# Kernel tuning notes

Hardware: AMD Instinct MI355X
Metric: run time of the kernel (lower is better)

The kernel has to match this reference:

```python
import jax, jax.numpy as jnp
import numpy as np

B, T, N, D = 256, 200, 8, 64
MODEL = N * D          # 512
FFN_H = 1024 * N // 4  # 2048
EPS = 1.1920929e-07    # torch.finfo(float32).eps (nn.RMSNorm default eps=None)


def setup_inputs() -> dict:
    key = jax.random.key(0)
    ks = jax.random.split(key, 9)
    def xavier(k, shape):
        fan_in, fan_out = shape[-2], shape[-1]
        lim = float(np.sqrt(6.0 / (fan_in + fan_out)))
        return jax.random.uniform(k, shape, jnp.float32, -lim, lim)
    q = jax.random.normal(ks[0], (B, N, D), jnp.float32)
    seq = jax.random.normal(ks[1], (B, T, MODEL), jnp.float32)
    seq_mask = jax.random.randint(ks[2], (B, T), 0, 2) > 0
    seq_mask = seq_mask.at[:, 0].set(True)  # ensure >=1 valid position per row
    return {
        "q": q,
        "seq": seq,
        "rms_w": jnp.ones((MODEL,), jnp.float32),
        "w1": xavier(ks[3], (MODEL, FFN_H)),
        "w2": xavier(ks[4], (MODEL, FFN_H)),
        "w3": xavier(ks[5], (FFN_H, MODEL)),
        "w_k": xavier(ks[6], (N, D, D)),
        "w_v": xavier(ks[7], (N, D, D)),
        "seq_mask": seq_mask,
    }


def reference(q, seq, rms_w, w1, w2, w3, w_k, w_v, seq_mask):
    # RMSNorm
    sn = seq * jax.lax.rsqrt(jnp.mean(seq * seq, axis=-1, keepdims=True) + EPS) * rms_w
    # SwiGLU FFN + residual (dropout=0 / eval)
    h = (jax.nn.silu(sn @ w1) * (sn @ w2)) @ w3 + seq  # (B,T,N*D)
    hh = h.reshape(B, T, N, D)
    keys = jnp.einsum('btnd,nde->bnte', hh, w_k)    # (B,N,T,D)
    values = jnp.einsum('btnd,nde->bnte', hh, w_v)  # (B,N,T,D)
    scale = D ** (-0.5)
    scores = jnp.einsum('bnd,bntd->bnt', q, keys) * scale  # single-query attention
    scores = jnp.where(seq_mask[:, None, :], scores, -jnp.inf)
    attn = jax.nn.softmax(scores, axis=-1)
    ctx = jnp.einsum('bnt,bntd->bnd', attn, values)
    return ctx + q
```

## Files before the change

kernel.cpp:

```cpp
#include <hip/hip_runtime.h>
#include <hip/hip_fp16.h>
#include <cstdint>
#include <cstddef>

typedef unsigned short u16t;
typedef __bf16 bf16x8 __attribute__((ext_vector_type(8)));
typedef float f32x4 __attribute__((ext_vector_type(4)));
typedef unsigned short u16x8 __attribute__((ext_vector_type(8)));

#define BT_ROWS 51200
#define MODEL 512
#define FFNH 2048

__device__ __forceinline__ float bf2f(u16t u) {
  union { unsigned int i; float f; } v; v.i = ((unsigned int)u) << 16; return v.f;
}
__device__ __forceinline__ u16t f2bf(float f) {
  union { float f; unsigned int i; } v; v.f = f;
  return (u16t)((v.i + 0x7fffu + ((v.i >> 16) & 1u)) >> 16);
}
__device__ __forceinline__ float ldf(const void* p, size_t i, int dt) {
  if (dt == 1) return ((const float*)p)[i];
  u16t u = ((const u16t*)p)[i];
  if (dt == 0) return bf2f(u);
  __half h; *(u16t*)&h = u; return __half2float(h);
}
__device__ __forceinline__ void stf(void* p, size_t i, int dt, float f) {
  if (dt == 1) { ((float*)p)[i] = f; }
  else if (dt == 0) { ((u16t*)p)[i] = f2bf(f); }
  else { __half h = __float2half(f); ((u16t*)p)[i] = *(u16t*)&h; }
}
__device__ __forceinline__ void gl2lds16(const void* g, void* l) {
  __builtin_amdgcn_global_load_lds((const __attribute__((address_space(1))) void*)g,
                                   (__attribute__((address_space(3))) void*)l, 16, 0, 0);
}

__global__ __launch_bounds__(256) void detect_dtype_k(const unsigned int* __restrict__ w1,
                                                      int* __restrict__ dflag) {
  __shared__ int sh[8];
  int a = 0, bc = 0;
  for (int it = 0; it < 64; it++) {
    unsigned int w = w1[it * 256 + threadIdx.x];
    u16t lo = (u16t)(w & 0xffffu), hi = (u16t)(w >> 16);
    float flo = bf2f(lo);
    a += (!(fabsf(flo) < 0.25f)) ? 1 : 0;
    __half hh; *(u16t*)&hh = hi; float fhi = __half2float(hh);
    bc += (fabsf(fhi) > 0.25f && fabsf(fhi) < 256.f) ? 1 : 0;
  }
#pragma unroll
  for (int o = 32; o; o >>= 1) { a += __shfl_xor(a, o); bc += __shfl_xor(bc, o); }
  int w = threadIdx.x >> 6;
  if ((threadIdx.x & 63) == 0) { sh[w] = a; sh[4 + w] = bc; }
  __syncthreads();
  if (threadIdx.x == 0) {
    int A = sh[0] + sh[1] + sh[2] + sh[3];
    int B = sh[4] + sh[5] + sh[6] + sh[7];
    dflag[0] = (A > 256) ? 1 : ((B < 256) ? 2 : 0);
  }
}

__global__ __launch_bounds__(256) void detect_mask_k(const unsigned int* __restrict__ msk,
                                                     int* __restrict__ flag) {
  int i = blockIdx.x * 256 + threadIdx.x;
  int bad = 0;
  if (i < 12800) bad = (msk[i] > 1u) ? 1 : 0;
  unsigned long long bl = __ballot(bad);
  if ((threadIdx.x & 63) == 0 && bl) atomicOr(flag, 1);
}

__global__ __launch_bounds__(256) void rmsnorm_k(const void* __restrict__ seq,
                                                 const void* __restrict__ w,
                                                 const int* __restrict__ dfp,
                                                 u16t* __restrict__ xn) {
  const int dt = dfp[0];
  int row = blockIdx.x * 4 + (threadIdx.x >> 6);
  int lane = threadIdx.x & 63;
  size_t base = (size_t)row * MODEL + lane * 8;
  float x[8]; float ss = 0.f;
  if (dt == 0) {
    u16x8 xv = *(const u16x8*)((const u16t*)seq + base);
#pragma unroll
    for (int j = 0; j < 8; j++) { x[j] = bf2f(xv[j]); ss += x[j] * x[j]; }
  } else if (dt == 1) {
    const f32x4* p = (const f32x4*)((const float*)seq + base);
    f32x4 va = p[0], vb = p[1];
#pragma unroll
    for (int j = 0; j < 4; j++) { x[j] = va[j]; x[4 + j] = vb[j]; }
#pragma unroll
    for (int j = 0; j < 8; j++) ss += x[j] * x[j];
  } else {
#pragma unroll
    for (int j = 0; j < 8; j++) { x[j] = ldf(seq, base + j, dt); ss += x[j] * x[j]; }
  }
#pragma unroll
  for (int o = 32; o; o >>= 1) ss += __shfl_xor(ss, o);
  float rstd = rsqrtf(ss * (1.f / 512.f) + 1.1920929e-07f);
  u16x8 ov;
#pragma unroll
  for (int j = 0; j < 8; j++) ov[j] = f2bf(x[j] * rstd * ldf(w, lane * 8 + j, dt));
  *(u16x8*)(xn + base) = ov;
}

__global__ __launch_bounds__(256) void transpose_k(const void* __restrict__ src,
                                                   u16t* __restrict__ dst,
                                                   const int* __restrict__ dfp,
                                                   int R, int C) {
  const int dt = dfp[0];
  __shared__ u16t tile[32][33];
  int x = threadIdx.x & 31, y = threadIdx.x >> 5;
  int c0 = blockIdx.x * 32, r0 = blockIdx.y * 32;
#pragma unroll
  for (int i = 0; i < 32; i += 8)
    tile[y + i][x] = f2bf(ldf(src, (size_t)(r0 + y + i) * C + c0 + x, dt));
  __syncthreads();
#pragma unroll
  for (int i = 0; i < 32; i += 8) dst[(size_t)(c0 + y + i) * R + r0 + x] = tile[x][y + i];
}


__global__ __launch_bounds__(256, 4) void ffn_gemm1(const u16t* __restrict__ Xn,
                                                    const u16t* __restrict__ W1t,
                                                    const u16t* __restrict__ W2t,
                                                    u16t* __restrict__ Act) {
  __shared__ u16t As[128 * 64];
  __shared__ u16t B1s[64 * 64];
  __shared__ u16t B2s[64 * 64];
  const int tid = threadIdx.x;
  const int lane = tid & 63;
  const int wave = tid >> 6;
  const int wr = wave >> 1, wc = wave & 1;
  const int quad = lane >> 4, l16 = lane & 15;
  const int nBase = blockIdx.x * 64;
  const int mBase = blockIdx.y * 128;
  const int wuBase = tid & ~63;

  f32x4 acc1[4][2], acc2[4][2];
  const f32x4 zf = {0.f, 0.f, 0.f, 0.f};
#pragma unroll
  for (int i = 0; i < 4; i++)
#pragma unroll
    for (int j = 0; j < 2; j++) { acc1[i][j] = zf; acc2[i][j] = zf; }

  for (int kt = 0; kt < MODEL; kt += 64) {
#pragma unroll
    for (int c = 0; c < 4; c++) {
      int chunk = c * 256 + tid;
      int r = chunk >> 3, k8 = (chunk & 7) ^ (r & 7);
      gl2lds16(Xn + (size_t)(mBase + r) * MODEL + kt + k8 * 8, As + (size_t)(c * 256 + wuBase) * 8);
    }
#pragma unroll
    for (int c = 0; c < 2; c++) {
      int chunk = c * 256 + tid;
      int r = chunk >> 3, k8 = (chunk & 7) ^ (r & 7);
      gl2lds16(W1t + (size_t)(nBase + r) * MODEL + kt + k8 * 8, B1s + (size_t)(c * 256 + wuBase) * 8);
      gl2lds16(W2t + (size_t)(nBase + r) * MODEL + kt + k8 * 8, B2s + (size_t)(c * 256 + wuBase) * 8);
    }
    __syncthreads();
#pragma unroll
    for (int ks = 0; ks < 64; ks += 32) {
      bf16x8 a[4], b1[2], b2[2];
      const int sw = (ks >> 3) + quad;
#pragma unroll
      for (int mi = 0; mi < 4; mi++) {
        int row = wr * 64 + mi * 16 + l16;
        a[mi] = *(const bf16x8*)(As + row * 64 + ((sw ^ (row & 7)) << 3));
      }
#pragma unroll
      for (int ni = 0; ni < 2; ni++) {
        int row = wc * 32 + ni * 16 + l16;
        b1[ni] = *(const bf16x8*)(B1s + row * 64 + ((sw ^ (row & 7)) << 3));
        b2[ni] = *(const bf16x8*)(B2s + row * 64 + ((sw ^ (row & 7)) << 3));
      }
#pragma unroll
      for (int mi = 0; mi < 4; mi++)
#pragma unroll
        for (int ni = 0; ni < 2; ni++) {
          acc1[mi][ni] = __builtin_amdgcn_mfma_f32_16x16x32_bf16(a[mi], b1[ni], acc1[mi][ni], 0, 0, 0);
          acc2[mi][ni] = __builtin_amdgcn_mfma_f32_16x16x32_bf16(a[mi], b2[ni], acc2[mi][ni], 0, 0, 0);
        }
    }
    __syncthreads();
  }
#pragma unroll
  for (int mi = 0; mi < 4; mi++)
#pragma unroll
    for (int ni = 0; ni < 2; ni++)
#pragma unroll
      for (int r = 0; r < 4; r++) {
        int row = mBase + wr * 64 + mi * 16 + quad * 4 + r;
        int col = nBase + wc * 32 + ni * 16 + l16;
        float g1 = acc1[mi][ni][r], g2 = acc2[mi][ni][r];
        float sl = g1 / (1.f + __expf(-g1));
        Act[(size_t)row * FFNH + col] = f2bf(sl * g2);
      }
}

__global__ __launch_bounds__(256, 4) void ffn_gemm2(const u16t* __restrict__ Act,
                                                    const u16t* __restrict__ W3t,
                                                    const void* __restrict__ Seq,
                                                    const int* __restrict__ dfp,
                                                    u16t* __restrict__ H, int rowOff) {
  __shared__ u16t As[128 * 64];
  __shared__ u16t Bs[128 * 64];
  const int dt = dfp[0];
  const int tid = threadIdx.x;
  const int lane = tid & 63;
  const int wave = tid >> 6;
  const int wr = wave >> 1, wc = wave & 1;
  const int quad = lane >> 4, l16 = lane & 15;
  const int nBase = blockIdx.x * 128;
  const int mBase = blockIdx.y * 128;
  const int wuBase = tid & ~63;

  f32x4 acc[4][4];
  const f32x4 zf = {0.f, 0.f, 0.f, 0.f};
#pragma unroll
  for (int i = 0; i < 4; i++)
#pragma unroll
    for (int j = 0; j < 4; j++) acc[i][j] = zf;

  for (int kt = 0; kt < FFNH; kt += 64) {
#pragma unroll
    for (int c = 0; c < 4; c++) {
      int chunk = c * 256 + tid;
      int r = chunk >> 3, k8 = (chunk & 7) ^ (r & 7);
      gl2lds16(Act + (size_t)(mBase + r) * FFNH + kt + k8 * 8, As + (size_t)(c * 256 + wuBase) * 8);
      gl2lds16(W3t + (size_t)(nBase + r) * FFNH + kt + k8 * 8, Bs + (size_t)(c * 256 + wuBase) * 8);
    }
    __syncthreads();
#pragma unroll
    for (int ks = 0; ks < 64; ks += 32) {
      bf16x8 a[4], b[4];
      const int sw = (ks >> 3) + quad;
#pragma unroll
      for (int mi = 0; mi < 4; mi++) {
        int row = wr * 64 + mi * 16 + l16;
        a[mi] = *(const bf16x8*)(As + row * 64 + ((sw ^ (row & 7)) << 3));
      }
#pragma unroll
      for (int ni = 0; ni < 4; ni++) {
        int row = wc * 64 + ni * 16 + l16;
        b[ni] = *(const bf16x8*)(Bs + row * 64 + ((sw ^ (row & 7)) << 3));
      }
#pragma unroll
      for (int mi = 0; mi < 4; mi++)
#pragma unroll
        for (int ni = 0; ni < 4; ni++)
          acc[mi][ni] = __builtin_amdgcn_mfma_f32_16x16x32_bf16(a[mi], b[ni], acc[mi][ni], 0, 0, 0);
    }
    __syncthreads();
  }
#pragma unroll
  for (int mi = 0; mi < 4; mi++)
#pragma unroll
    for (int ni = 0; ni < 4; ni++)
#pragma unroll
      for (int r = 0; r < 4; r++) {
        int grow = rowOff + mBase + wr * 64 + mi * 16 + quad * 4 + r;
        int col = nBase + wc * 64 + ni * 16 + l16;
        float v = acc[mi][ni][r] + ldf(Seq, (size_t)grow * MODEL + col, dt);
        H[(size_t)grow * MODEL + col] = f2bf(v);
      }
}

__global__ __launch_bounds__(256) void attn_k(const u16t* __restrict__ H,
                                              const void* __restrict__ q,
                                              const void* __restrict__ wk,
                                              const void* __restrict__ wv,
                                              const int* __restrict__ mask,
                                              const int* __restrict__ mflagp,
                                              const int* __restrict__ dfp,
                                              void* __restrict__ out) {
  const int b = blockIdx.x >> 3;
  const int n = blockIdx.x & 7;
  const int tid = threadIdx.x;
  const int w = tid >> 6;
  const int lane = tid & 63;
  const int T = 200;
  const int HS = 66;
  const int dt = dfp[0];
  const int mflag = mflagp[0];

  __shared__ u16t hbuf[200 * HS];
  __shared__ float qk[64];
  __shared__ float sc[200];
  __shared__ float part[256];
  __shared__ float red[8];
  __shared__ float ctx[64];

  for (int chunk = tid; chunk < 1600; chunk += 256) {
    int r = chunk >> 3, c = (chunk & 7) << 3;
    u16x8 v = *(const u16x8*)(H + (size_t)(b * 200 + r) * MODEL + n * 64 + c);
#pragma unroll
    for (int j = 0; j < 8; j++) hbuf[r * HS + c + j] = v[j];
  }

  {
    int d = tid >> 2, sub = tid & 3;
    float s = 0.f;
    size_t wb = ((size_t)n * 64 + d) * 64 + sub * 16;
    size_t qb = (size_t)(b * 8 + n) * 64 + sub * 16;
#pragma unroll
    for (int i = 0; i < 16; i++) s += ldf(wk, wb + i, dt) * ldf(q, qb + i, dt);
    part[tid] = s;
  }
  __syncthreads();
  if (tid < 64) qk[tid] = part[tid * 4] + part[tid * 4 + 1] + part[tid * 4 + 2] + part[tid * 4 + 3];
  __syncthreads();

  float sv = -INFINITY;
  if (tid < T) {
    float s = 0.f;
#pragma unroll 16
    for (int d = 0; d < 64; d++) s += bf2f(hbuf[tid * HS + d]) * qk[d];
    int mv = mflag ? (int)((const unsigned char*)mask)[b * 200 + tid] : mask[b * 200 + tid];
    sv = mv ? s * 0.125f : -INFINITY;
  }

  float mx = sv;
#pragma unroll
  for (int o = 32; o; o >>= 1) mx = fmaxf(mx, __shfl_xor(mx, o));
  if (lane == 0) red[w] = mx;
  __syncthreads();
  float gmax = fmaxf(fmaxf(red[0], red[1]), fmaxf(red[2], red[3]));
  float e = 0.f;
  if (gmax == -INFINITY) {
    if (tid == 0) e = 1.f;
  } else if (tid < T) {
    e = __expf(sv - gmax);
  }
  float s = e;
#pragma unroll
  for (int o = 32; o; o >>= 1) s += __shfl_xor(s, o);
  if (lane == 0) red[4 + w] = s;
  __syncthreads();
  float inv = 1.f / (red[4] + red[5] + red[6] + red[7]);
  if (tid < T) sc[tid] = e * inv;
  __syncthreads();

  float a2 = 0.f;
  for (int t = w; t < T; t += 4) a2 += sc[t] * bf2f(hbuf[t * HS + lane]);
  part[tid] = a2;
  __syncthreads();
  if (tid < 64) ctx[tid] = part[tid] + part[64 + tid] + part[128 + tid] + part[192 + tid];
  __syncthreads();

  {
    int od = tid & 63;
    float s2 = 0.f;
#pragma unroll
    for (int i = 0; i < 16; i++) {
      int d = w * 16 + i;
      s2 += ctx[d] * ldf(wv, ((size_t)n * 64 + d) * 64 + od, dt);
    }
    part[tid] = s2;
  }
  __syncthreads();
  if (tid < 64) {
    size_t oi = (size_t)(b * 8 + n) * 64 + tid;
    stf(out, oi, dt,
        part[tid] + part[64 + tid] + part[128 + tid] + part[192 + tid] + ldf(q, oi, dt));
  }
}

extern "C" void kernel_launch(void* const* d_in, const int* in_sizes, int n_in,
                              void* d_out, int out_size, void* d_ws, size_t ws_size,
                              hipStream_t stream) {
  (void)in_sizes; (void)n_in; (void)out_size;
  const void* q   = d_in[0];
  const void* seq = d_in[1];
  const void* rw  = d_in[2];
  const void* w1  = d_in[3];
  const void* w2  = d_in[4];
  const void* w3  = d_in[5];
  const void* wk  = d_in[6];
  const void* wv  = d_in[7];
  const int*  msk = (const int*)d_in[8];

  char* ws = (char*)d_ws;
  size_t off = 0;
  auto alloc = [&](size_t b) { void* p = ws + off; off = (off + b + 255) & ~(size_t)255; return p; };
  int*  flags = (int*)alloc(512);
  int*  mflag = flags + 0;
  int*  dflag = flags + 4;
  u16t* Xn  = (u16t*)alloc((size_t)BT_ROWS * MODEL * 2);
  u16t* W1t = (u16t*)alloc((size_t)FFNH * MODEL * 2);
  u16t* W2t = (u16t*)alloc((size_t)FFNH * MODEL * 2);
  u16t* W3t = (u16t*)alloc((size_t)MODEL * FFNH * 2);
  size_t actBytes = (ws_size > off) ? (ws_size - off) : 0;
  long tpc = (long)(actBytes / ((size_t)128 * FFNH * 2));
  if (tpc < 1) tpc = 1;
  if (tpc > 200) tpc = 200;
  u16t* ActB = (u16t*)(ws + off);

  hipMemsetAsync(flags, 0, 512, stream);
  detect_dtype_k<<<dim3(1), dim3(256), 0, stream>>>((const unsigned int*)w1, dflag);
  detect_mask_k<<<dim3(50), dim3(256), 0, stream>>>((const unsigned int*)msk, mflag);

  rmsnorm_k<<<dim3(BT_ROWS / 4), dim3(256), 0, stream>>>(seq, rw, dflag, Xn);
  transpose_k<<<dim3(FFNH / 32, MODEL / 32), dim3(256), 0, stream>>>(w1, W1t, dflag, MODEL, FFNH);
  transpose_k<<<dim3(FFNH / 32, MODEL / 32), dim3(256), 0, stream>>>(w2, W2t, dflag, MODEL, FFNH);
  transpose_k<<<dim3(MODEL / 32, FFNH / 32), dim3(256), 0, stream>>>(w3, W3t, dflag, FFNH, MODEL);

  for (int t0 = 0; t0 < 400; t0 += (int)tpc) {
    int tiles = (400 - t0 < (int)tpc) ? (400 - t0) : (int)tpc;
    int rows0 = t0 * 128;
    ffn_gemm1<<<dim3(FFNH / 64, tiles), dim3(256), 0, stream>>>(
        Xn + (size_t)rows0 * MODEL, W1t, W2t, ActB);
    ffn_gemm2<<<dim3(MODEL / 128, tiles), dim3(256), 0, stream>>>(
        ActB, W3t, seq, dflag, Xn, rows0);
  }
  attn_k<<<dim3(2048), dim3(256), 0, stream>>>(Xn, q, wk, wv, msk, mflag, dflag, d_out);
}
```

Measured before the change: 696.1 us.

## Fold W3 and attention projections algebraically to skip second FFN GEMM

Drops the Act@W3 GEMM and the materialized H tensor. Scores are computed directly as Act·(W3·Wk·q) plus seq·(Wk·q), using a precomputed per-batch w3qk vector. Context is accumulated over Act and seq with the softmax weights, then projected through W3 and Wv afterwards. This cuts the large 2048x512 GEMM over all rows in exchange for per-batch fp32 dot products and a w3qk workspace. The chunk size is also aligned to whole batches, and the dtype probe reads fewer samples.

```diff
diff --git a/kernel.cpp b/kernel.cpp
--- a/kernel.cpp
+++ b/kernel.cpp
@@ -7,6 +7,7 @@
 typedef __bf16 bf16x8 __attribute__((ext_vector_type(8)));
 typedef float f32x4 __attribute__((ext_vector_type(4)));
 typedef unsigned short u16x8 __attribute__((ext_vector_type(8)));
+typedef unsigned short u16x4 __attribute__((ext_vector_type(4)));
 
 #define BT_ROWS 51200
 #define MODEL 512
@@ -38,9 +39,13 @@
 __global__ __launch_bounds__(256) void detect_dtype_k(const unsigned int* __restrict__ w1,
                                                       int* __restrict__ dflag) {
   __shared__ int sh[8];
+  unsigned int wb[8];
+#pragma unroll
+  for (int it = 0; it < 8; it++) wb[it] = w1[it * 256 + threadIdx.x];
   int a = 0, bc = 0;
-  for (int it = 0; it < 64; it++) {
-    unsigned int w = w1[it * 256 + threadIdx.x];
+#pragma unroll
+  for (int it = 0; it < 8; it++) {
+    unsigned int w = wb[it];
     u16t lo = (u16t)(w & 0xffffu), hi = (u16t)(w >> 16);
     float flo = bf2f(lo);
     a += (!(fabsf(flo) < 0.25f)) ? 1 : 0;
@@ -55,7 +60,7 @@
   if (threadIdx.x == 0) {
     int A = sh[0] + sh[1] + sh[2] + sh[3];
     int B = sh[4] + sh[5] + sh[6] + sh[7];
-    dflag[0] = (A > 256) ? 1 : ((B < 256) ? 2 : 0);
+    dflag[0] = (A > 128) ? 1 : ((B < 128) ? 2 : 0);
   }
 }
 
@@ -117,6 +122,47 @@
   for (int i = 0; i < 32; i += 8) dst[(size_t)(c0 + y + i) * R + r0 + x] = tile[x][y + i];
 }
 
+__global__ __launch_bounds__(256) void cast_w3_k(const void* __restrict__ w3,
+                                                 const int* __restrict__ dfp,
+                                                 u16t* __restrict__ w3bf) {
+  const int dt = dfp[0];
+  size_t i = (size_t)blockIdx.x * 256 + threadIdx.x;
+  w3bf[i] = f2bf(ldf(w3, i, dt));
+}
+
+__global__ __launch_bounds__(64) void qk_k(const void* __restrict__ q,
+                                           const void* __restrict__ wk,
+                                           const int* __restrict__ dfp,
+                                           float* __restrict__ qkg) {
+  const int dt = dfp[0];
+  int bn = blockIdx.x;
+  int n = bn & 7, d = threadIdx.x;
+  float s = 0.f;
+#pragma unroll 8
+  for (int e = 0; e < 64; e++)
+    s += ldf(wk, ((size_t)(n * 64 + d) << 6) + e, dt) * ldf(q, ((size_t)bn << 6) + e, dt);
+  qkg[((size_t)bn << 6) + d] = s;
+}
+
+__global__ __launch_bounds__(256) void w3qk_k(const void* __restrict__ w3,
+                                              const float* __restrict__ qkg,
+                                              const int* __restrict__ dfp,
+                                              float* __restrict__ w3qk) {
+  const int dt = dfp[0];
+  const int n = blockIdx.x;
+  const int k = blockIdx.y * 256 + threadIdx.x;
+  const int bh = blockIdx.z;
+  float w3row[64];
+#pragma unroll 16
+  for (int d = 0; d < 64; d++) w3row[d] = ldf(w3, ((size_t)k << 9) + n * 64 + d, dt);
+  for (int b = bh * 128; b < bh * 128 + 128; b++) {
+    const float* qp = qkg + ((size_t)(b * 8 + n) << 6);
+    float s = 0.f;
+#pragma unroll 16
+    for (int d = 0; d < 64; d++) s += w3row[d] * qp[d];
+    w3qk[((size_t)(n * 256 + b) << 11) + k] = s;
+  }
+}
 
 __global__ __launch_bounds__(256, 4) void ffn_gemm1(const u16t* __restrict__ Xn,
                                                     const u16t* __restrict__ W1t,
@@ -195,172 +241,148 @@
       }
 }
 
-__global__ __launch_bounds__(256, 4) void ffn_gemm2(const u16t* __restrict__ Act,
-                                                    const u16t* __restrict__ W3t,
-                                                    const void* __restrict__ Seq,
-                                                    const int* __restrict__ dfp,
-                                                    u16t* __restrict__ H, int rowOff) {
-  __shared__ u16t As[128 * 64];
-  __shared__ u16t Bs[128 * 64];
-  const int dt = dfp[0];
-  const int tid = threadIdx.x;
-  const int lane = tid & 63;
-  const int wave = tid >> 6;
-  const int wr = wave >> 1, wc = wave & 1;
-  const int quad = lane >> 4, l16 = lane & 15;
-  const int nBase = blockIdx.x * 128;
-  const int mBase = blockIdx.y * 128;
-  const int wuBase = tid & ~63;
-
-  f32x4 acc[4][4];
-  const f32x4 zf = {0.f, 0.f, 0.f, 0.f};
-#pragma unroll
-  for (int i = 0; i < 4; i++)
-#pragma unroll
-    for (int j = 0; j < 4; j++) acc[i][j] = zf;
-
-  for (int kt = 0; kt < FFNH; kt += 64) {
-#pragma unroll
-    for (int c = 0; c < 4; c++) {
-      int chunk = c * 256 + tid;
-      int r = chunk >> 3, k8 = (chunk & 7) ^ (r & 7);
-      gl2lds16(Act + (size_t)(mBase + r) * FFNH + kt + k8 * 8, As + (size_t)(c * 256 + wuBase) * 8);
-      gl2lds16(W3t + (size_t)(nBase + r) * FFNH + kt + k8 * 8, Bs + (size_t)(c * 256 + wuBase) * 8);
-    }
-    __syncthreads();
-#pragma unroll
-    for (int ks = 0; ks < 64; ks += 32) {
-      bf16x8 a[4], b[4];
-      const int sw = (ks >> 3) + quad;
-#pragma unroll
-      for (int mi = 0; mi < 4; mi++) {
-        int row = wr * 64 + mi * 16 + l16;
-        a[mi] = *(const bf16x8*)(As + row * 64 + ((sw ^ (row & 7)) << 3));
+__global__ __launch_bounds__(512) void scores_k(const u16t* __restrict__ ActB,
+                                                const void* __restrict__ seq,
+                                                const float* __restrict__ qkg,
+                                                const float* __restrict__ w3qk,
+                                                const int* __restrict__ mask,
+                                                const int* __restrict__ mflagp,
+                                                const int* __restrict__ dfp,
+                                                float* __restrict__ sc, int b0) {
+  const int dt = dfp[0], mflag = mflagp[0];
+  const int bl = blockIdx.x, bg = b0 + bl;
+  const int th = blockIdx.y;
+  const int tid = threadIdx.x, wave = tid >> 6, lane = tid & 63;
+  __shared__ float wq[8][2048];
+#pragma unroll
+  for (int n = 0; n < 8; n++)
+#pragma unroll
+    for (int i = 0; i < 4; i++)
+      wq[n][i * 512 + tid] = w3qk[((size_t)(n * 256 + bg) << 11) + i * 512 + tid];
+  __syncthreads();
+  const int ns = lane >> 3;
+  const float* qp = qkg + ((size_t)(bg * 8 + ns) << 6) + (lane & 7) * 8;
+  for (int ti = wave; ti < 100; ti += 8) {
+    int t = th * 100 + ti;
+    const u16t* ar = ActB + ((size_t)(bl * 200 + t) << 11);
+    float acc[8] = {0.f, 0.f, 0.f, 0.f, 0.f, 0.f, 0.f, 0.f};
+#pragma unroll
+    for (int i = 0; i < 8; i++) {
+      int k = i * 256 + lane * 4;
+      u16x4 a4 = *(const u16x4*)(ar + k);
+      float a0 = bf2f(a4[0]), a1 = bf2f(a4[1]), a2 = bf2f(a4[2]), a3 = bf2f(a4[3]);
+#pragma unroll
+      for (int n = 0; n < 8; n++) {
+        f32x4 wv4 = *(const f32x4*)&wq[n][k];
+        acc[n] += a0 * wv4[0] + a1 * wv4[1] + a2 * wv4[2] + a3 * wv4[3];
       }
-#pragma unroll
-      for (int ni = 0; ni < 4; ni++) {
-        int row = wc * 64 + ni * 16 + l16;
-        b[ni] = *(const bf16x8*)(Bs + row * 64 + ((sw ^ (row & 7)) << 3));
-      }
-#pragma unroll
-      for (int mi = 0; mi < 4; mi++)
-#pragma unroll
-        for (int ni = 0; ni < 4; ni++)
-          acc[mi][ni] = __builtin_amdgcn_mfma_f32_16x16x32_bf16(a[mi], b[ni], acc[mi][ni], 0, 0, 0);
-    }
-    __syncthreads();
-  }
-#pragma unroll
-  for (int mi = 0; mi < 4; mi++)
-#pragma unroll
-    for (int ni = 0; ni < 4; ni++)
-#pragma unroll
-      for (int r = 0; r < 4; r++) {
-        int grow = rowOff + mBase + wr * 64 + mi * 16 + quad * 4 + r;
-        int col = nBase + wc * 64 + ni * 16 + l16;
-        float v = acc[mi][ni][r] + ldf(Seq, (size_t)grow * MODEL + col, dt);
-        H[(size_t)grow * MODEL + col] = f2bf(v);
-      }
-}
-
-__global__ __launch_bounds__(256) void attn_k(const u16t* __restrict__ H,
-                                              const void* __restrict__ q,
-                                              const void* __restrict__ wk,
-                                              const void* __restrict__ wv,
-                                              const int* __restrict__ mask,
-                                              const int* __restrict__ mflagp,
-                                              const int* __restrict__ dfp,
-                                              void* __restrict__ out) {
-  const int b = blockIdx.x >> 3;
-  const int n = blockIdx.x & 7;
-  const int tid = threadIdx.x;
-  const int w = tid >> 6;
-  const int lane = tid & 63;
-  const int T = 200;
-  const int HS = 66;
-  const int dt = dfp[0];
-  const int mflag = mflagp[0];
-
-  __shared__ u16t hbuf[200 * HS];
-  __shared__ float qk[64];
-  __shared__ float sc[200];
-  __shared__ float part[256];
-  __shared__ float red[8];
-  __shared__ float ctx[64];
-
-  for (int chunk = tid; chunk < 1600; chunk += 256) {
-    int r = chunk >> 3, c = (chunk & 7) << 3;
-    u16x8 v = *(const u16x8*)(H + (size_t)(b * 200 + r) * MODEL + n * 64 + c);
-#pragma unroll
-    for (int j = 0; j < 8; j++) hbuf[r * HS + c + j] = v[j];
-  }
+    }
+    float sq = 0.f;
+    size_t sb = ((size_t)(bg * 200 + t) << 9) + lane * 8;
+    if (dt == 1) {
+      const float* sp = (const float*)seq + sb;
+      f32x4 s0 = *(const f32x4*)sp, s1 = *(const f32x4*)(sp + 4);
+      sq = s0[0] * qp[0] + s0[1] * qp[1] + s0[2] * qp[2] + s0[3] * qp[3]
+         + s1[0] * qp[4] + s1[1] * qp[5] + s1[2] * qp[6] + s1[3] * qp[7];
+    } else {
+#pragma unroll
+      for (int j = 0; j < 8; j++) sq += ldf(seq, sb + j, dt) * qp[j];
+    }
+    sq += __shfl_xor(sq, 1); sq += __shfl_xor(sq, 2); sq += __shfl_xor(sq, 4);
+#pragma unroll
+    for (int n = 0; n < 8; n++)
+#pragma unroll
+      for (int o = 32; o; o >>= 1) acc[n] += __shfl_xor(acc[n], o);
+    if ((lane & 7) == 0) {
+      float sco = (acc[ns] + sq) * 0.125f;
+      int mv = mflag ? (int)((const unsigned char*)mask)[bg * 200 + t] : mask[bg * 200 + t];
+      sc[(size_t)(bg * 8 + ns) * 200 + t] = mv ? sco : -INFINITY;
+    }
+  }
+}
+
+__global__ __launch_bounds__(512) void ctx_k(const u16t* __restrict__ ActB,
+                                             const void* __restrict__ seq,
+                                             const void* __restrict__ q,
+                                             const void* __restrict__ wv,
+                                             const u16t* __restrict__ w3bf,
+                                             const float* __restrict__ sc,
+                                             const int* __restrict__ dfp,
+                                             int b0, void* __restrict__ out) {
+  const int dt = dfp[0];
+  const int bl = blockIdx.x, bg = b0 + bl;
+  const int tid = threadIdx.x, wave = tid >> 6, lane = tid & 63;
+  __shared__ float p_lds[8][200];
+  __shared__ float ctxa[8][2048];
+  __shared__ float ch[512];
 
   {
-    int d = tid >> 2, sub = tid & 3;
-    float s = 0.f;
-    size_t wb = ((size_t)n * 64 + d) * 64 + sub * 16;
-    size_t qb = (size_t)(b * 8 + n) * 64 + sub * 16;
-#pragma unroll
-    for (int i = 0; i < 16; i++) s += ldf(wk, wb + i, dt) * ldf(q, qb + i, dt);
-    part[tid] = s;
-  }
-  __syncthreads();
-  if (tid < 64) qk[tid] = part[tid * 4] + part[tid * 4 + 1] + part[tid * 4 + 2] + part[tid * 4 + 3];
-  __syncthreads();
-
-  float sv = -INFINITY;
-  if (tid < T) {
-    float s = 0.f;
-#pragma unroll 16
-    for (int d = 0; d < 64; d++) s += bf2f(hbuf[tid * HS + d]) * qk[d];
-    int mv = mflag ? (int)((const unsigned char*)mask)[b * 200 + tid] : mask[b * 200 + tid];
-    sv = mv ? s * 0.125f : -INFINITY;
-  }
-
-  float mx = sv;
-#pragma unroll
-  for (int o = 32; o; o >>= 1) mx = fmaxf(mx, __shfl_xor(mx, o));
-  if (lane == 0) red[w] = mx;
-  __syncthreads();
-  float gmax = fmaxf(fmaxf(red[0], red[1]), fmaxf(red[2], red[3]));
-  float e = 0.f;
-  if (gmax == -INFINITY) {
-    if (tid == 0) e = 1.f;
-  } else if (tid < T) {
-    e = __expf(sv - gmax);
-  }
-  float s = e;
-#pragma unroll
-  for (int o = 32; o; o >>= 1) s += __shfl_xor(s, o);
-  if (lane == 0) red[4 + w] = s;
-  __syncthreads();
-  float inv = 1.f / (red[4] + red[5] + red[6] + red[7]);
-  if (tid < T) sc[tid] = e * inv;
-  __syncthreads();
-
-  float a2 = 0.f;
-  for (int t = w; t < T; t += 4) a2 += sc[t] * bf2f(hbuf[t * HS + lane]);
-  part[tid] = a2;
-  __syncthreads();
-  if (tid < 64) ctx[tid] = part[tid] + part[64 + tid] + part[128 + tid] + part[192 + tid];
-  __syncthreads();
-
+    int n = wave;
+    float v[4];
+#pragma unroll
+    for (int r = 0; r < 4; r++) {
+      int t = r * 64 + lane;
+      v[r] = (t < 200) ? sc[(size_t)(bg * 8 + n) * 200 + t] : -INFINITY;
+    }
+    float mx = fmaxf(fmaxf(v[0], v[1]), fmaxf(v[2], v[3]));
+#pragma unroll
+    for (int o = 32; o; o >>= 1) mx = fmaxf(mx, __shfl_xor(mx, o));
+    float s = 0.f, e[4];
+#pragma unroll
+    for (int r = 0; r < 4; r++) {
+      int t = r * 64 + lane;
+      if (mx == -INFINITY) e[r] = (t == 0) ? 1.f : 0.f;
+      else e[r] = (t < 200) ? __expf(v[r] - mx) : 0.f;
+      s += e[r];
+    }
+#pragma unroll
+    for (int o = 32; o; o >>= 1) s += __shfl_xor(s, o);
+    float inv = 1.f / s;
+#pragma unroll
+    for (int r = 0; r < 4; r++) { int t = r * 64 + lane; if (t < 200) p_lds[n][t] = e[r] * inv; }
+  }
+  __syncthreads();
+
+  float acc[8][4] = {};
+  float accs = 0.f;
+  for (int t = 0; t < 200; t++) {
+    u16x4 a4 = *(const u16x4*)(ActB + ((size_t)(bl * 200 + t) << 11) + tid * 4);
+    float a0 = bf2f(a4[0]), a1 = bf2f(a4[1]), a2 = bf2f(a4[2]), a3 = bf2f(a4[3]);
+#pragma unroll
+    for (int n = 0; n < 8; n++) {
+      float pv = p_lds[n][t];
+      acc[n][0] += pv * a0; acc[n][1] += pv * a1; acc[n][2] += pv * a2; acc[n][3] += pv * a3;
+    }
+    float svv = ldf(seq, ((size_t)(bg * 200 + t) << 9) + tid, dt);
+    accs += p_lds[wave][t] * svv;
+  }
+#pragma unroll
+  for (int n = 0; n < 8; n++) {
+    f32x4 v4 = {acc[n][0], acc[n][1], acc[n][2], acc[n][3]};
+    *(f32x4*)&ctxa[n][tid * 4] = v4;
+  }
+  __syncthreads();
+
+  float chv = accs;
   {
-    int od = tid & 63;
-    float s2 = 0.f;
-#pragma unroll
-    for (int i = 0; i < 16; i++) {
-      int d = w * 16 + i;
-      s2 += ctx[d] * ldf(wv, ((size_t)n * 64 + d) * 64 + od, dt);
-    }
-    part[tid] = s2;
-  }
-  __syncthreads();
-  if (tid < 64) {
-    size_t oi = (size_t)(b * 8 + n) * 64 + tid;
-    stf(out, oi, dt,
-        part[tid] + part[64 + tid] + part[128 + tid] + part[192 + tid] + ldf(q, oi, dt));
-  }
+    const u16t* wr = w3bf + wave * 64 + lane;
+    for (int k4 = 0; k4 < 512; k4++) {
+      f32x4 c4 = *(const f32x4*)&ctxa[wave][k4 * 4];
+      chv += c4[0] * bf2f(wr[(size_t)(k4 * 4 + 0) * 512])
+           + c4[1] * bf2f(wr[(size_t)(k4 * 4 + 1) * 512])
+           + c4[2] * bf2f(wr[(size_t)(k4 * 4 + 2) * 512])
+           + c4[3] * bf2f(wr[(size_t)(k4 * 4 + 3) * 512]);
+    }
+  }
+  ch[tid] = chv;
+  __syncthreads();
+
+  float o = 0.f;
+#pragma unroll 8
+  for (int d = 0; d < 64; d++)
+    o += ch[wave * 64 + d] * ldf(wv, ((size_t)(wave * 64 + d) << 6) + lane, dt);
+  size_t oi = (size_t)(bg * 8 + wave) * 64 + lane;
+  stf(out, oi, dt, o + ldf(q, oi, dt));
 }
 
 extern "C" void kernel_launch(void* const* d_in, const int* in_sizes, int n_in,
@@ -380,17 +402,22 @@
   char* ws = (char*)d_ws;
   size_t off = 0;
   auto alloc = [&](size_t b) { void* p = ws + off; off = (off + b + 255) & ~(size_t)255; return p; };
-  int*  flags = (int*)alloc(512);
-  int*  mflag = flags + 0;
-  int*  dflag = flags + 4;
-  u16t* Xn  = (u16t*)alloc((size_t)BT_ROWS * MODEL * 2);
-  u16t* W1t = (u16t*)alloc((size_t)FFNH * MODEL * 2);
-  u16t* W2t = (u16t*)alloc((size_t)FFNH * MODEL * 2);
-  u16t* W3t = (u16t*)alloc((size_t)MODEL * FFNH * 2);
+  int*   flags = (int*)alloc(512);
+  int*   mflag = flags + 0;
+  int*   dflag = flags + 4;
+  u16t*  Xn    = (u16t*)alloc((size_t)BT_ROWS * MODEL * 2);
+  u16t*  W1t   = (u16t*)alloc((size_t)FFNH * MODEL * 2);
+  u16t*  W2t   = (u16t*)alloc((size_t)FFNH * MODEL * 2);
+  u16t*  W3bf  = (u16t*)alloc((size_t)FFNH * MODEL * 2);
+  float* qkg   = (float*)alloc((size_t)256 * 8 * 64 * 4);
+  float* w3qk  = (float*)alloc((size_t)8 * 256 * FFNH * 4);
+  float* scb   = (float*)alloc((size_t)256 * 8 * 200 * 4);
   size_t actBytes = (ws_size > off) ? (ws_size - off) : 0;
-  long tpc = (long)(actBytes / ((size_t)128 * FFNH * 2));
-  if (tpc < 1) tpc = 1;
-  if (tpc > 200) tpc = 200;
+  size_t unitB = (size_t)25 * 128 * FFNH * 2;
+  long units = (long)(actBytes / unitB);
+  if (units < 1) units = 1;
+  if (units > 8) units = 8;
+  int tpc = (int)units * 25;
   u16t* ActB = (u16t*)(ws + off);
 
   hipMemsetAsync(flags, 0, 512, stream);
@@ -400,15 +427,18 @@
   rmsnorm_k<<<dim3(BT_ROWS / 4), dim3(256), 0, stream>>>(seq, rw, dflag, Xn);
   transpose_k<<<dim3(FFNH / 32, MODEL / 32), dim3(256), 0, stream>>>(w1, W1t, dflag, MODEL, FFNH);
   transpose_k<<<dim3(FFNH / 32, MODEL / 32), dim3(256), 0, stream>>>(w2, W2t, dflag, MODEL, FFNH);
-  transpose_k<<<dim3(MODEL / 32, FFNH / 32), dim3(256), 0, stream>>>(w3, W3t, dflag, FFNH, MODEL);
-
-  for (int t0 = 0; t0 < 400; t0 += (int)tpc) {
-    int tiles = (400 - t0 < (int)tpc) ? (400 - t0) : (int)tpc;
+  cast_w3_k<<<dim3(4096), dim3(256), 0, stream>>>(w3, dflag, W3bf);
+  qk_k<<<dim3(2048), dim3(64), 0, stream>>>(q, wk, dflag, qkg);
+  w3qk_k<<<dim3(8, 8, 2), dim3(256), 0, stream>>>(w3, qkg, dflag, w3qk);
+
+  for (int t0 = 0; t0 < 400; t0 += tpc) {
+    int tiles = (400 - t0 < tpc) ? (400 - t0) : tpc;
     int rows0 = t0 * 128;
+    int b0 = rows0 / 200;
+    int bc = tiles * 128 / 200;
     ffn_gemm1<<<dim3(FFNH / 64, tiles), dim3(256), 0, stream>>>(
         Xn + (size_t)rows0 * MODEL, W1t, W2t, ActB);
-    ffn_gemm2<<<dim3(MODEL / 128, tiles), dim3(256), 0, stream>>>(
-        ActB, W3t, seq, dflag, Xn, rows0);
-  }
-  attn_k<<<dim3(2048), dim3(256), 0, stream>>>(Xn, q, wk, wv, msk, mflag, dflag, d_out);
-}
+    scores_k<<<dim3(bc, 2), dim3(512), 0, stream>>>(ActB, seq, qkg, w3qk, msk, mflag, dflag, scb, b0);
+    ctx_k<<<dim3(bc), dim3(512), 0, stream>>>(ActB, seq, q, wv, W3bf, scb, dflag, b0, d_out);
+  }
+}
```

Result: slower. 1.343 ms (+93.0%).
